# Kernel tuning notes

Hardware: AMD Instinct MI355X
Metric: run time of the kernel (lower is better)

The kernel has to match this reference:

```python
import jax, jax.numpy as jnp
import numpy as np

N_ATOMS = 1_000_000
N_MOL = 50_000
NF = 128


def setup_inputs() -> dict:
    key = jax.random.key(0)
    ks = jax.random.split(key, 10)
    inp = {
        "charges": jax.random.normal(ks[0], (N_ATOMS, 1), dtype=jnp.float32),
        "f0": jax.random.normal(ks[1], (N_ATOMS, NF), dtype=jnp.float32),
        "f1": jax.random.normal(ks[2], (N_ATOMS, NF), dtype=jnp.float32),
        "f2": jax.random.normal(ks[3], (N_ATOMS, NF), dtype=jnp.float32),
        "mol_index": jnp.sort(jax.random.randint(ks[4], (N_ATOMS,), 0, N_MOL, dtype=jnp.int64) if jax.config.jax_enable_x64 else jax.random.randint(ks[4], (N_ATOMS,), 0, N_MOL).astype(jnp.int32)),
        "n_molecules": N_MOL,
        # Linear(nf, 1) params; first layer has bias=first_is_interacting=False.
        "w0": jax.random.normal(ks[5], (NF,), dtype=jnp.float32) / np.sqrt(NF),
        "w1": jax.random.normal(ks[6], (NF,), dtype=jnp.float32) / np.sqrt(NF),
        "w2": jax.random.normal(ks[7], (NF,), dtype=jnp.float32) / np.sqrt(NF),
        "b1": jax.random.normal(ks[8], (), dtype=jnp.float32) * 0.01,
        "b2": jax.random.normal(ks[9], (), dtype=jnp.float32) * 0.01,
    }
    return inp


def reference(charges, f0, f1, f2, mol_index, n_molecules, w0, w1, w2, b1, b2):
    # Per-term nf->1 projections, summed. [n_atoms, 1]
    total_lin = (f0 @ w0 + (f1 @ w1 + b1) + (f2 @ w2 + b2))[:, None]
    # Source bug (reproduced faithfully): quad terms also use layers_lin,
    # so total_quad == total_lin.
    total_quad = total_lin
    atom_charge_energy = (total_quad * charges) ** 2 + total_lin
    molecule_charge_energy = jax.ops.segment_sum(
        atom_charge_energy, mol_index, num_segments=n_molecules
    )
    return (molecule_charge_energy, atom_charge_energy)
```

## Files before the change

### kernel.cpp

```cpp
#include <hip/hip_runtime.h>


__global__ void zero_kernel(float* __restrict__ p, int n) {
    int i = blockIdx.x * blockDim.x + threadIdx.x;
    if (i < n) p[i] = 0.0f;
}

__global__ void __launch_bounds__(256)
charge_energy_kernel(const float* __restrict__ charges,
                     const float* __restrict__ f0,
                     const float* __restrict__ f1,
                     const float* __restrict__ f2,
                     const int*   __restrict__ mol_index,
                     const float* __restrict__ w0,
                     const float* __restrict__ w1,
                     const float* __restrict__ w2,
                     const float* __restrict__ b1p,
                     const float* __restrict__ b2p,
                     float* __restrict__ mol_out,
                     float* __restrict__ atom_out,
                     int n_atoms)
{
    const int lane32  = threadIdx.x & 31;
    const int group   = threadIdx.x >> 5;
    const int gpb     = blockDim.x >> 5;
    const float bias  = b1p[0] + b2p[0];

    const float4 w0c = reinterpret_cast<const float4*>(w0)[lane32];
    const float4 w1c = reinterpret_cast<const float4*>(w1)[lane32];
    const float4 w2c = reinterpret_cast<const float4*>(w2)[lane32];

    for (long long atom = (long long)blockIdx.x * gpb + group;
         atom < n_atoms;
         atom += (long long)gridDim.x * gpb) {

        const long long row = atom * 128;
        const float4 a0 = reinterpret_cast<const float4*>(f0 + row)[lane32];
        const float4 a1 = reinterpret_cast<const float4*>(f1 + row)[lane32];
        const float4 a2 = reinterpret_cast<const float4*>(f2 + row)[lane32];

        float partial = a0.x * w0c.x + a0.y * w0c.y + a0.z * w0c.z + a0.w * w0c.w
                      + a1.x * w1c.x + a1.y * w1c.y + a1.z * w1c.z + a1.w * w1c.w
                      + a2.x * w2c.x + a2.y * w2c.y + a2.z * w2c.z + a2.w * w2c.w;

        #pragma unroll
        for (int m = 16; m >= 1; m >>= 1)
            partial += __shfl_xor(partial, m, 64);

        if (lane32 == 0) {
            const float lin = partial + bias;
            const float c   = charges[atom];
            const float lc  = lin * c;
            const float e   = lc * lc + lin;
            atom_out[atom] = e;
            atomicAdd(&mol_out[mol_index[atom]], e);
        }
    }
}

extern "C" void kernel_launch(void* const* d_in, const int* in_sizes, int n_in,
                              void* d_out, int out_size, void* d_ws, size_t ws_size,
                              hipStream_t stream) {
    const float* charges   = (const float*)d_in[0];
    const float* f0        = (const float*)d_in[1];
    const float* f1        = (const float*)d_in[2];
    const float* f2        = (const float*)d_in[3];
    const int*   mol_index = (const int*)  d_in[4];
    const float* w0        = (const float*)d_in[6];
    const float* w1        = (const float*)d_in[7];
    const float* w2        = (const float*)d_in[8];
    const float* b1p       = (const float*)d_in[9];
    const float* b2p       = (const float*)d_in[10];

    const int n_atoms = in_sizes[0];
    const int n_mol   = out_size - n_atoms;

    float* mol_out  = (float*)d_out;
    float* atom_out = mol_out + n_mol;

    {
        int blocks = (n_mol + 255) / 256;
        hipLaunchKernelGGL(zero_kernel, dim3(blocks), dim3(256), 0, stream,
                           mol_out, n_mol);
    }

    const int blocks = 2048;
    hipLaunchKernelGGL(charge_energy_kernel, dim3(blocks), dim3(256), 0, stream,
                       charges, f0, f1, f2, mol_index, w0, w1, w2, b1p, b2p,
                       mol_out, atom_out, n_atoms);
}
```

Baseline: 310.7 us.

## Assign contiguous atom chunks per wave and run-length merge segment atomics

```diff
diff --git a/kernel.cpp b/kernel.cpp
--- a/kernel.cpp
+++ b/kernel.cpp
@@ -19,43 +19,70 @@
                      const float* __restrict__ b2p,
                      float* __restrict__ mol_out,
                      float* __restrict__ atom_out,
-                     int n_atoms)
+                     int n_atoms,
+                     int chunk)
 {
-    const int lane32  = threadIdx.x & 31;
-    const int group   = threadIdx.x >> 5;
-    const int gpb     = blockDim.x >> 5;
-    const float bias  = b1p[0] + b2p[0];
+    const int lane   = threadIdx.x & 63;
+    const int lane32 = lane & 31;
+    const long long wid = (long long)blockIdx.x * (blockDim.x >> 6) + (threadIdx.x >> 6);
 
+    long long a0 = wid * (long long)chunk;
+    if (a0 >= n_atoms) return;
+    long long a1 = a0 + chunk;
+    if (a1 > n_atoms) a1 = n_atoms;
+
+    const float bias = b1p[0] + b2p[0];
     const float4 w0c = reinterpret_cast<const float4*>(w0)[lane32];
     const float4 w1c = reinterpret_cast<const float4*>(w1)[lane32];
     const float4 w2c = reinterpret_cast<const float4*>(w2)[lane32];
 
-    for (long long atom = (long long)blockIdx.x * gpb + group;
-         atom < n_atoms;
-         atom += (long long)gridDim.x * gpb) {
+    int   cur_mol = -1;
+    float cur_sum = 0.0f;
 
-        const long long row = atom * 128;
-        const float4 a0 = reinterpret_cast<const float4*>(f0 + row)[lane32];
-        const float4 a1 = reinterpret_cast<const float4*>(f1 + row)[lane32];
-        const float4 a2 = reinterpret_cast<const float4*>(f2 + row)[lane32];
+    for (long long a = a0; a < a1; a += 2) {
+        const float2 cc = *reinterpret_cast<const float2*>(charges + a);
+        const int2   mm = *reinterpret_cast<const int2*>(mol_index + a);
 
-        float partial = a0.x * w0c.x + a0.y * w0c.y + a0.z * w0c.z + a0.w * w0c.w
-                      + a1.x * w1c.x + a1.y * w1c.y + a1.z * w1c.z + a1.w * w1c.w
-                      + a2.x * w2c.x + a2.y * w2c.y + a2.z * w2c.z + a2.w * w2c.w;
+        const float4 x0 = (reinterpret_cast<const float4*>(f0) + a * 32)[lane];
+        const float4 x1 = (reinterpret_cast<const float4*>(f1) + a * 32)[lane];
+        const float4 x2 = (reinterpret_cast<const float4*>(f2) + a * 32)[lane];
+
+        float partial = x0.x * w0c.x + x0.y * w0c.y + x0.z * w0c.z + x0.w * w0c.w
+                      + x1.x * w1c.x + x1.y * w1c.y + x1.z * w1c.z + x1.w * w1c.w
+                      + x2.x * w2c.x + x2.y * w2c.y + x2.z * w2c.z + x2.w * w2c.w;
 
         #pragma unroll
         for (int m = 16; m >= 1; m >>= 1)
             partial += __shfl_xor(partial, m, 64);
 
-        if (lane32 == 0) {
-            const float lin = partial + bias;
-            const float c   = charges[atom];
-            const float lc  = lin * c;
-            const float e   = lc * lc + lin;
-            atom_out[atom] = e;
-            atomicAdd(&mol_out[mol_index[atom]], e);
+        const float sA = __shfl(partial, 0, 64);
+        const float sB = __shfl(partial, 32, 64);
+
+        if (lane == 0) {
+            const float lin0 = sA + bias;
+            const float lin1 = sB + bias;
+            const float t0 = lin0 * cc.x;
+            const float t1 = lin1 * cc.y;
+            const float e0 = t0 * t0 + lin0;
+            const float e1 = t1 * t1 + lin1;
+            *reinterpret_cast<float2*>(atom_out + a) = make_float2(e0, e1);
+
+            if (mm.x != cur_mol) {
+                if (cur_mol >= 0) atomicAdd(&mol_out[cur_mol], cur_sum);
+                cur_mol = mm.x; cur_sum = e0;
+            } else {
+                cur_sum += e0;
+            }
+            if (mm.y != cur_mol) {
+                atomicAdd(&mol_out[cur_mol], cur_sum);
+                cur_mol = mm.y; cur_sum = e1;
+            } else {
+                cur_sum += e1;
+            }
         }
     }
+    if (lane == 0 && cur_mol >= 0)
+        atomicAdd(&mol_out[cur_mol], cur_sum);
 }
 
 extern "C" void kernel_launch(void* const* d_in, const int* in_sizes, int n_in,
@@ -84,8 +111,12 @@
                            mol_out, n_mol);
     }
 
-    const int blocks = 2048;
+    const int blocks  = 2048;
+    const int n_waves = blocks * (256 / 64);
+    int chunk = (n_atoms + n_waves - 1) / n_waves;
+    chunk = (chunk + 1) & ~1;
+
     hipLaunchKernelGGL(charge_energy_kernel, dim3(blocks), dim3(256), 0, stream,
                        charges, f0, f1, f2, mol_index, w0, w1, w2, b1p, b2p,
-                       mol_out, atom_out, n_atoms);
+                       mol_out, atom_out, n_atoms, chunk);
 }
```

New measurement: 308.9 us. Within noise of the previous version (-0.6%).
